# Kernel tuning notes

Hardware: AMD Instinct MI355X
Metric: run time of the kernel (lower is better)

Reference implementation:

```python
import jax, jax.numpy as jnp
import numpy as np

EPS = 1e-6
WEIGHTS = dict(segmentation=1.0, absence=2.0, attention_supervision=0.3,
               confidence=0.1, dice=1.0, false_positive_suppression=0.5)


def setup_inputs() -> dict:
    key = jax.random.key(0)
    ks = jax.random.split(key, 6)
    B, S, H, W = 8, 12, 512, 512
    seg_logits = jax.random.normal(ks[0], (B, S, H, W), dtype=jnp.float32)
    seg_probs = jax.nn.sigmoid(jax.random.normal(ks[1], (B, S, H, W), dtype=jnp.float32))
    seg_targets = (jax.random.uniform(ks[2], (B, S, H, W)) < 0.3).astype(jnp.float32)
    presence_probs = jnp.clip(jax.random.uniform(ks[3], (B, S)), 1e-6, 1.0 - 1e-6)
    presence_targets = (jax.random.uniform(ks[4], (B, S)) < 0.7).astype(jnp.float32)
    attention_maps = jnp.clip(jax.random.uniform(ks[5], (B, S, H, W)), 1e-6, 1.0 - 1e-6)
    return {"seg_logits": seg_logits, "seg_probs": seg_probs,
            "presence_probs": presence_probs, "attention_maps": attention_maps,
            "seg_targets": seg_targets, "presence_targets": presence_targets}


def _bce(p, t):
    # torch BCELoss: -(t*log(p) + (1-t)*log(1-p)), logs clamped to >= -100
    return -(t * jnp.clip(jnp.log(p), -100.0, None)
             + (1.0 - t) * jnp.clip(jnp.log1p(-p), -100.0, None))


def _bce_with_logits(x, t):
    # stable: max(x,0) - x*t + log(1+exp(-|x|))
    return jnp.maximum(x, 0.0) - x * t + jnp.log1p(jnp.exp(-jnp.abs(x)))


def reference(seg_logits, seg_probs, presence_probs, attention_maps,
              seg_targets, presence_targets):
    B, S = presence_targets.shape
    mask = presence_targets != 0          # [B,S] present structures
    maskf = mask.astype(seg_logits.dtype)
    n_valid = maskf.sum()
    n_absent = (1.0 - maskf).sum()

    # per-(b,s) segmentation BCE (mean over spatial)
    seg_bce_bs = _bce_with_logits(seg_logits, seg_targets).mean(axis=(-2, -1))  # [B,S]
    # per-(b,s) dice loss (each original call is on a [1,1,...] slice)
    inter = jnp.sum(seg_probs * seg_targets, axis=(-2, -1))
    psum = jnp.sum(seg_probs, axis=(-2, -1))
    tsum = jnp.sum(seg_targets, axis=(-2, -1))
    dice_bs = 1.0 - (2.0 * inter + EPS) / (psum + tsum + EPS)                   # [B,S]

    seg_loss = jnp.where(n_valid > 0, jnp.sum(seg_bce_bs * maskf) / jnp.maximum(n_valid, 1.0), 0.0)
    dice_loss = jnp.where(n_valid > 0, jnp.sum(dice_bs * maskf) / jnp.maximum(n_valid, 1.0), 0.0)

    # false positive suppression on absent structures
    fp_bs = jnp.maximum(seg_probs, 0.0).mean(axis=(-2, -1))                     # [B,S]
    fp_loss = jnp.where(n_absent > 0,
                        jnp.sum(fp_bs * (1.0 - maskf)) / jnp.maximum(n_absent, 1.0), 0.0)

    # presence/absence BCE over all (b,s)
    absence_loss = _bce(presence_probs, presence_targets).mean()

    # attention supervision on present structures, normalized by B*S
    att_target = (seg_targets > 0.5).astype(seg_targets.dtype)
    att_bce_bs = _bce(attention_maps, att_target).mean(axis=(-2, -1))           # [B,S]
    att_loss = jnp.sum(att_bce_bs * maskf) / (B * S)

    # confidence calibration penalty
    p, t = presence_probs, presence_targets
    conf = (jnp.where((t == 0) & (p > 0.5), (p - 0.5) ** 2, 0.0)
            + jnp.where((t == 1) & (p < 0.5), (0.5 - p) ** 2, 0.0))
    conf_loss = conf.sum() / (B * S)

    total = (WEIGHTS['segmentation'] * seg_loss + WEIGHTS['dice'] * dice_loss
             + WEIGHTS['absence'] * absence_loss
             + WEIGHTS['attention_supervision'] * att_loss
             + WEIGHTS['confidence'] * conf_loss
             + WEIGHTS['false_positive_suppression'] * fp_loss)

    return jnp.stack([total, seg_loss, dice_loss, absence_loss,
                      att_loss, conf_loss, fp_loss])
```

## Files before the change

kernel.cpp:

```cpp
#include <hip/hip_runtime.h>
#include <hip/hip_bf16.h>


constexpr int kB = 8, kS = 12, kH = 512, kW = 512;
constexpr int kSlices = kB * kS;
constexpr long kHW = (long)kH * kW;
constexpr int kVecPerSlice = (int)(kHW / 4);
constexpr int kBlocksPerSlice = 128;
constexpr int kBlock = 256;
constexpr int kVecPerBlock = kVecPerSlice / kBlocksPerSlice;
constexpr float kEPS = 1e-6f;
constexpr float kLOG2E = 1.44269504088896340736f;
constexpr float kLN2 = 0.69314718055994530942f;


__global__ __launch_bounds__(kBlock) void slice_reduce_kernel(
    const float4* __restrict__ logits,
    const float4* __restrict__ probs,
    const float4* __restrict__ att,
    const float4* __restrict__ tgt,
    float* __restrict__ partial) {
  const int gid = blockIdx.x;
  const int slice = gid >> 7;
  const int chunk = gid & (kBlocksPerSlice - 1);
  const long base = (long)slice * kVecPerSlice + (long)chunk * kVecPerBlock
                    + threadIdx.x;

  const float4 x0 = logits[base];
  const float4 x1 = logits[base + kBlock];
  const float4 p0 = probs[base];
  const float4 p1 = probs[base + kBlock];
  const float4 a0 = att[base];
  const float4 a1 = att[base + kBlock];
  const float4 t0 = tgt[base];
  const float4 t1 = tgt[base + kBlock];

  float s_bce = 0.f, s_inter = 0.f, s_p = 0.f, s_t = 0.f, s_fp = 0.f,
        s_att = 0.f;

  const float xs[8] = {x0.x, x0.y, x0.z, x0.w, x1.x, x1.y, x1.z, x1.w};
  const float ps[8] = {p0.x, p0.y, p0.z, p0.w, p1.x, p1.y, p1.z, p1.w};
  const float as[8] = {a0.x, a0.y, a0.z, a0.w, a1.x, a1.y, a1.z, a1.w};
  const float ts[8] = {t0.x, t0.y, t0.z, t0.w, t1.x, t1.y, t1.z, t1.w};

#pragma unroll
  for (int j = 0; j < 8; ++j) {
    const float x = xs[j], p = ps[j], a = as[j], t = ts[j];
    const float u = __builtin_amdgcn_exp2f(-fabsf(x) * kLOG2E);
    s_bce += fmaxf(x, 0.f) - x * t + kLN2 * __builtin_amdgcn_logf(1.f + u);
    s_inter += p * t;
    s_p += p;
    s_t += t;
    s_fp += fmaxf(p, 0.f);
    const float c = (t > 0.5f) ? a : 1.0f - a;
    s_att -= kLN2 * __builtin_amdgcn_logf(c);
  }

  float vals[6] = {s_bce, s_inter, s_p, s_t, s_fp, s_att};
  const int lane = threadIdx.x & 63;
  const int wave = threadIdx.x >> 6;
  __shared__ float lds[4][6];
#pragma unroll
  for (int q = 0; q < 6; ++q) {
    float v = vals[q];
    for (int off = 32; off > 0; off >>= 1) v += __shfl_down(v, off, 64);
    if (lane == 0) lds[wave][q] = v;
  }
  __syncthreads();
  if (threadIdx.x == 0) {
#pragma unroll
    for (int q = 0; q < 6; ++q) {
      const float v = lds[0][q] + lds[1][q] + lds[2][q] + lds[3][q];
      atomicAdd(&partial[slice * 6 + q], v);
    }
  }
}

__global__ __launch_bounds__(128) void finalize_kernel(
    const float* __restrict__ partial,
    const float* __restrict__ pprobs,
    const float* __restrict__ ptgt,
    float* __restrict__ out) {
  const int i = threadIdx.x;
  __shared__ float acc[7][128];
  float q[7] = {0.f, 0.f, 0.f, 0.f, 0.f, 0.f, 0.f};
  if (i < kSlices) {
    const float t = ptgt[i];
    const float m = (t != 0.f) ? 1.f : 0.f;
    const float inv = 1.f / (float)kHW;
    const float bce = partial[i * 6 + 0] * inv;
    const float inter = partial[i * 6 + 1];
    const float psum = partial[i * 6 + 2];
    const float tsum = partial[i * 6 + 3];
    const float fp = partial[i * 6 + 4] * inv;
    const float attv = partial[i * 6 + 5] * inv;
    const float dice = 1.f - (2.f * inter + kEPS) / (psum + tsum + kEPS);
    q[0] = bce * m;
    q[1] = dice * m;
    q[2] = fp * (1.f - m);
    q[3] = attv * m;
    const float p = pprobs[i];
    q[4] = -(t * fmaxf(logf(p), -100.f) +
             (1.f - t) * fmaxf(log1pf(-p), -100.f));
    float c = 0.f;
    if (t == 0.f && p > 0.5f) c += (p - 0.5f) * (p - 0.5f);
    if (t == 1.f && p < 0.5f) c += (0.5f - p) * (0.5f - p);
    q[5] = c;
    q[6] = m;
  }
#pragma unroll
  for (int k = 0; k < 7; ++k) acc[k][i] = q[k];
  __syncthreads();
  if (i == 0) {
    float s[7];
#pragma unroll
    for (int k = 0; k < 7; ++k) {
      float v = 0.f;
      for (int j = 0; j < kSlices; ++j) v += acc[k][j];
      s[k] = v;
    }
    const float n_valid = s[6];
    const float n_absent = (float)kSlices - n_valid;
    const float seg_loss = (n_valid > 0.f) ? s[0] / fmaxf(n_valid, 1.f) : 0.f;
    const float dice_loss = (n_valid > 0.f) ? s[1] / fmaxf(n_valid, 1.f) : 0.f;
    const float fp_loss = (n_absent > 0.f) ? s[2] / fmaxf(n_absent, 1.f) : 0.f;
    const float att_loss = s[3] / (float)kSlices;
    const float absence_loss = s[4] / (float)kSlices;
    const float conf_loss = s[5] / (float)kSlices;
    const float total = 1.0f * seg_loss + 1.0f * dice_loss +
                        2.0f * absence_loss + 0.3f * att_loss +
                        0.1f * conf_loss + 0.5f * fp_loss;
    out[0] = total;
    out[1] = seg_loss;
    out[2] = dice_loss;
    out[3] = absence_loss;
    out[4] = att_loss;
    out[5] = conf_loss;
    out[6] = fp_loss;
  }
}

extern "C" void kernel_launch(void* const* d_in, const int* in_sizes, int n_in,
                              void* d_out, int out_size, void* d_ws,
                              size_t ws_size, hipStream_t stream) {
  const float4* seg_logits = (const float4*)d_in[0];
  const float4* seg_probs = (const float4*)d_in[1];
  const float* presence_probs = (const float*)d_in[2];
  const float4* attention_maps = (const float4*)d_in[3];
  const float4* seg_targets = (const float4*)d_in[4];
  const float* presence_targets = (const float*)d_in[5];
  float* out = (float*)d_out;
  float* partial = (float*)d_ws;

  hipMemsetAsync(partial, 0, kSlices * 6 * sizeof(float), stream);

  slice_reduce_kernel<<<kSlices * kBlocksPerSlice, kBlock, 0, stream>>>(
      seg_logits, seg_probs, attention_maps, seg_targets, partial);
  finalize_kernel<<<1, 128, 0, stream>>>(partial, presence_probs,
                                         presence_targets, out);
}
```

Measured before the change: 401.5 us.

## Use fewer blocks per slice with a software-prefetched streaming loop

Cuts blocks per slice from 128 to 16, so each thread now walks 16 float4 groups per input instead of 2. The loop loads the next iteration's four float4 values while it computes the current ones, and a launch_bounds occupancy hint is added. This is meant to reduce block launch, reduction and atomic overhead and to keep memory requests in flight. In exchange there are far fewer blocks (1536), which may leave some latency exposed on a large GPU.

Measured after the change: 481.5 us. +19.9%, slower.

```diff
diff --git a/kernel.cpp b/kernel.cpp
--- a/kernel.cpp
+++ b/kernel.cpp
@@ -6,54 +6,62 @@
 constexpr int kSlices = kB * kS;
 constexpr long kHW = (long)kH * kW;
 constexpr int kVecPerSlice = (int)(kHW / 4);
-constexpr int kBlocksPerSlice = 128;
+constexpr int kBlocksPerSlice = 16;
 constexpr int kBlock = 256;
 constexpr int kVecPerBlock = kVecPerSlice / kBlocksPerSlice;
+constexpr int kIters = kVecPerBlock / kBlock;
 constexpr float kEPS = 1e-6f;
 constexpr float kLOG2E = 1.44269504088896340736f;
 constexpr float kLN2 = 0.69314718055994530942f;
 
 
-__global__ __launch_bounds__(kBlock) void slice_reduce_kernel(
+__global__ __launch_bounds__(kBlock, 6) void slice_reduce_kernel(
     const float4* __restrict__ logits,
     const float4* __restrict__ probs,
     const float4* __restrict__ att,
     const float4* __restrict__ tgt,
     float* __restrict__ partial) {
   const int gid = blockIdx.x;
-  const int slice = gid >> 7;
+  const int slice = gid >> 4;
   const int chunk = gid & (kBlocksPerSlice - 1);
   const long base = (long)slice * kVecPerSlice + (long)chunk * kVecPerBlock
                     + threadIdx.x;
 
-  const float4 x0 = logits[base];
-  const float4 x1 = logits[base + kBlock];
-  const float4 p0 = probs[base];
-  const float4 p1 = probs[base + kBlock];
-  const float4 a0 = att[base];
-  const float4 a1 = att[base + kBlock];
-  const float4 t0 = tgt[base];
-  const float4 t1 = tgt[base + kBlock];
-
   float s_bce = 0.f, s_inter = 0.f, s_p = 0.f, s_t = 0.f, s_fp = 0.f,
         s_att = 0.f;
 
-  const float xs[8] = {x0.x, x0.y, x0.z, x0.w, x1.x, x1.y, x1.z, x1.w};
-  const float ps[8] = {p0.x, p0.y, p0.z, p0.w, p1.x, p1.y, p1.z, p1.w};
-  const float as[8] = {a0.x, a0.y, a0.z, a0.w, a1.x, a1.y, a1.z, a1.w};
-  const float ts[8] = {t0.x, t0.y, t0.z, t0.w, t1.x, t1.y, t1.z, t1.w};
+  float4 cx = logits[base];
+  float4 cp = probs[base];
+  float4 ca = att[base];
+  float4 ct = tgt[base];
 
 #pragma unroll
-  for (int j = 0; j < 8; ++j) {
-    const float x = xs[j], p = ps[j], a = as[j], t = ts[j];
-    const float u = __builtin_amdgcn_exp2f(-fabsf(x) * kLOG2E);
-    s_bce += fmaxf(x, 0.f) - x * t + kLN2 * __builtin_amdgcn_logf(1.f + u);
-    s_inter += p * t;
-    s_p += p;
-    s_t += t;
-    s_fp += fmaxf(p, 0.f);
-    const float c = (t > 0.5f) ? a : 1.0f - a;
-    s_att -= kLN2 * __builtin_amdgcn_logf(c);
+  for (int k = 0; k < kIters; ++k) {
+    float4 nx, np, na, nt;
+    if (k + 1 < kIters) {
+      const long idx = base + (long)(k + 1) * kBlock;
+      nx = logits[idx];
+      np = probs[idx];
+      na = att[idx];
+      nt = tgt[idx];
+    }
+    const float xs[4] = {cx.x, cx.y, cx.z, cx.w};
+    const float ps[4] = {cp.x, cp.y, cp.z, cp.w};
+    const float as[4] = {ca.x, ca.y, ca.z, ca.w};
+    const float ts[4] = {ct.x, ct.y, ct.z, ct.w};
+#pragma unroll
+    for (int j = 0; j < 4; ++j) {
+      const float x = xs[j], p = ps[j], a = as[j], t = ts[j];
+      const float u = __builtin_amdgcn_exp2f(-fabsf(x) * kLOG2E);
+      s_bce += fmaxf(x, 0.f) - x * t + kLN2 * __builtin_amdgcn_logf(1.f + u);
+      s_inter += p * t;
+      s_p += p;
+      s_t += t;
+      s_fp += fmaxf(p, 0.f);
+      const float c = (t > 0.5f) ? a : 1.0f - a;
+      s_att -= kLN2 * __builtin_amdgcn_logf(c);
+    }
+    cx = nx; cp = np; ca = na; ct = nt;
   }
 
   float vals[6] = {s_bce, s_inter, s_p, s_t, s_fp, s_att};
```
